# Kernel optimization log

Hardware: AMD Instinct MI355X
Metric: run time of the kernel (lower is better)

Reference implementation:

```python
import jax, jax.numpy as jnp
import numpy as np

EMBED_DIM = 1024
NUM_HEADS = 16
HEAD_DIM = EMBED_DIM // NUM_HEADS


def setup_inputs() -> dict:
    key = jax.random.key(0)
    ks = jax.random.split(key, 7)
    B, S, D = 2, 2048, EMBED_DIM
    scale = 1.0 / np.sqrt(D)
    return {
        "query": jax.random.normal(ks[0], (B, S, D), dtype=jnp.float32),
        "key": jax.random.normal(ks[1], (B, S, D), dtype=jnp.float32),
        "value": jax.random.normal(ks[2], (B, S, D), dtype=jnp.float32),
        "W_qkv": jax.random.normal(ks[3], (D, 3 * D), dtype=jnp.float32) * scale,
        "b_qkv": jnp.zeros((3 * D,), dtype=jnp.float32),
        "W_out": jax.random.normal(ks[4], (D, D), dtype=jnp.float32) * scale,
        "b_out": jnp.zeros((D,), dtype=jnp.float32),
    }


def reference(query, key, value, W_qkv, b_qkv, W_out, b_out):
    # NOTE: the original torch forward ignores `key` and `value` — q,k,v all
    # come from qkv_proj(query). We keep them as args for signature fidelity.
    B, S, D = query.shape
    H, hd = NUM_HEADS, HEAD_DIM
    scale = hd ** -0.5

    qkv = query @ W_qkv + b_qkv                      # [B, S, 3D]
    qkv = qkv.reshape(B, S, 3, H, hd)
    q = jnp.transpose(qkv[:, :, 0], (0, 2, 1, 3))    # [B, H, S, hd]
    k = jnp.transpose(qkv[:, :, 1], (0, 2, 1, 3))
    v = jnp.transpose(qkv[:, :, 2], (0, 2, 1, 3))

    scores = jnp.einsum("bhsd,bhtd->bhst", q, k) * scale  # [B, H, S, S]
    attn = jax.nn.softmax(scores, axis=-1)
    out = jnp.einsum("bhst,bhtd->bhsd", attn, v)           # [B, H, S, hd]
    out = jnp.transpose(out, (0, 2, 1, 3)).reshape(B, S, D)
    return out @ W_out + b_out
```

## Files before the change

kernel.cpp:

```cpp
#include <hip/hip_runtime.h>
#include <stdint.h>

#define DEV static __device__ __forceinline__

typedef __attribute__((ext_vector_type(4))) float f32x4;
typedef __attribute__((ext_vector_type(16))) float f32x16;
typedef __attribute__((ext_vector_type(8))) short bf16x8;
typedef bf16x8 __attribute__((may_alias)) bf16x8_a;
typedef __attribute__((ext_vector_type(2))) unsigned int u32x2;
typedef u32x2 __attribute__((may_alias)) u32x2_a;

DEV unsigned short f2bf(float f) {
  union { float f; unsigned int u; } v; v.f = f;
  return (unsigned short)((v.u + 0x7FFFu + ((v.u >> 16) & 1u)) >> 16);
}

DEV float bf2f(unsigned short s) {
  union { unsigned int u; float f; } v; v.u = ((unsigned int)s) << 16;
  return v.f;
}

DEV float fast_exp2(float x) {
  float r;
  asm("v_exp_f32 %0, %1" : "=v"(r) : "v"(x));
  return r;
}

DEV unsigned int pktrunc(float lo, float hi) {
  union { float f; unsigned int u; } a, b; a.f = lo; b.f = hi;
  return __builtin_amdgcn_perm(b.u, a.u, 0x07060302u);
}

DEV void gload_lds16(const void* g, void* l) {
  __builtin_amdgcn_global_load_lds(
      (const __attribute__((address_space(1))) unsigned int*)g,
      (__attribute__((address_space(3))) unsigned int*)l, 16, 0, 0);
}

__global__ void cast_bf16_k(const float4* __restrict__ in, ushort4* __restrict__ out, int n4) {
  int i = blockIdx.x * 256 + threadIdx.x;
  if (i >= n4) return;
  float4 f = in[i];
  ushort4 o; o.x = f2bf(f.x); o.y = f2bf(f.y); o.z = f2bf(f.z); o.w = f2bf(f.w);
  out[i] = o;
}

__global__ __launch_bounds__(256) void transpose_bf16_k(const float* __restrict__ in,
                                                        unsigned short* __restrict__ out,
                                                        int R, int C) {
  __shared__ float tile[32][33];
  const int t = threadIdx.x;
  const int r = t >> 3, c4 = (t & 7) << 2;
  const int tr = blockIdx.y << 5, tc = blockIdx.x << 5;
  const float4 v = *(const float4*)(in + (size_t)(tr + r) * C + tc + c4);
  tile[r][c4] = v.x; tile[r][c4 + 1] = v.y; tile[r][c4 + 2] = v.z; tile[r][c4 + 3] = v.w;
  __syncthreads();
  ushort4 o;
  o.x = f2bf(tile[c4][r]); o.y = f2bf(tile[c4 + 1][r]);
  o.z = f2bf(tile[c4 + 2][r]); o.w = f2bf(tile[c4 + 3][r]);
  *(ushort4*)(out + (size_t)(tc + r) * R + tr + c4) = o;
}

template <int EPI, int BN>
__global__ __launch_bounds__(256) void gemm_bt(const unsigned short* __restrict__ A,
                                               const unsigned short* __restrict__ BT,
                                               const float* __restrict__ bias,
                                               float* __restrict__ Cout,
                                               unsigned short* __restrict__ q_buf,
                                               unsigned short* __restrict__ k_buf,
                                               unsigned short* __restrict__ vT_buf,
                                               int M, int N, int K) {
  constexpr int MI = (BN == 128) ? 4 : 2;
  constexpr int MW = MI * 16;
  __shared__ unsigned short As[2][128 * 32];
  __shared__ unsigned short Bs[2][BN * 32];
  const int t = threadIdx.x, w = t >> 6, l = t & 63;
  const int wm = (BN == 128) ? (w >> 1) : w;
  const int wn = (BN == 128) ? (w & 1) : 0;
  const int lg = l >> 4, ln = l & 15;

  const int xcd = blockIdx.x & 7, jb = blockIdx.x >> 3;
  const int m0 = (xcd * 4 + (jb & 3)) * 128;
  const int n0 = (jb >> 2) * BN;

  const int srow = w * 16 + (l >> 2);
  const int schunk = (l & 3) ^ ((l >> 3) & 3);
  const int dchunk = l & 3;

  f32x4 acc[MI][4] = {};

#define STAGE_G(buf, k0)                                                                              \
  do {                                                                                                \
    gload_lds16(A + (size_t)(m0 + srow) * K + (k0) + schunk * 8, &As[buf][srow * 32 + dchunk * 8]);   \
    gload_lds16(A + (size_t)(m0 + srow + 64) * K + (k0) + schunk * 8,                                 \
                &As[buf][(srow + 64) * 32 + dchunk * 8]);                                             \
    gload_lds16(BT + (size_t)(n0 + srow) * K + (k0) + schunk * 8, &Bs[buf][srow * 32 + dchunk * 8]);  \
    if (BN == 128)                                                                                    \
      gload_lds16(BT + (size_t)(n0 + srow + 64) * K + (k0) + schunk * 8,                              \
                  &Bs[buf][(srow + 64) * 32 + dchunk * 8]);                                           \
  } while (0)

  STAGE_G(0, 0);
  __syncthreads();

  const int rsw = (ln >> 1) & 3;
  const int rchunk = (lg ^ rsw) << 3;
  const int nit = K >> 5;
  for (int it = 0; it < nit; ++it) {
    const int buf = it & 1;
    if (it + 1 < nit) STAGE_G(buf ^ 1, (it + 1) * 32);

    bf16x8 af[MI], bfr[4];
#pragma unroll
    for (int mi = 0; mi < MI; ++mi)
      af[mi] = *(const bf16x8_a*)&As[buf][(wm * MW + mi * 16 + ln) * 32 + rchunk];
#pragma unroll
    for (int ni = 0; ni < 4; ++ni)
      bfr[ni] = *(const bf16x8_a*)&Bs[buf][(wn * 64 + ni * 16 + ln) * 32 + rchunk];
#pragma unroll
    for (int mi = 0; mi < MI; ++mi)
#pragma unroll
      for (int ni = 0; ni < 4; ++ni)
        acc[mi][ni] = __builtin_amdgcn_mfma_f32_16x16x32_bf16(af[mi], bfr[ni], acc[mi][ni], 0, 0, 0);

    __syncthreads();
  }
#undef STAGE_G

#pragma unroll
  for (int ni = 0; ni < 4; ++ni) {
    const int c = n0 + wn * 64 + ni * 16 + ln;
    const float bv = bias[c];
    if (EPI == 1) {
      const int which = c >> 10;
      const int h = (c >> 6) & 15;
      const int d = c & 63;
#pragma unroll
      for (int mi = 0; mi < MI; ++mi) {
        const int mrow = m0 + wm * MW + mi * 16 + lg * 4;
        const int b = mrow >> 11, s = mrow & 2047;
        const size_t bh = (size_t)(b * 16 + h);
        f32x4 v = acc[mi][ni];
        if (which == 0) {
          const float QSCALE = 0.125f * 1.44269504088896340736f;
          unsigned short* dst = q_buf + (bh * 2048 + s) * 64 + d;
#pragma unroll
          for (int r = 0; r < 4; ++r) dst[(size_t)r * 64] = f2bf((v[r] + bv) * QSCALE);
        } else if (which == 1) {
          unsigned short* dst = k_buf + (bh * 2048 + s) * 64 + d;
#pragma unroll
          for (int r = 0; r < 4; ++r) dst[(size_t)r * 64] = f2bf(v[r] + bv);
        } else {
          const int sp = (s & ~12) | ((s & 4) << 1) | ((s & 8) >> 1);
          unsigned short* dst = vT_buf + (bh * 64 + d) * 2048 + sp;
          ushort4 o4;
          o4.x = f2bf(v[0] + bv); o4.y = f2bf(v[1] + bv); o4.z = f2bf(v[2] + bv); o4.w = f2bf(v[3] + bv);
          *(ushort4*)dst = o4;
        }
      }
    } else {
#pragma unroll
      for (int mi = 0; mi < MI; ++mi) {
        const int mrow = m0 + wm * MW + mi * 16 + lg * 4;
        f32x4 v = acc[mi][ni];
#pragma unroll
        for (int r = 0; r < 4; ++r) Cout[(size_t)(mrow + r) * N + c] = v[r] + bv;
      }
    }
  }
}

template <int SPLIT>
__global__ __launch_bounds__(256, 4) void attn_k(const unsigned short* __restrict__ Qb,
                                                 const unsigned short* __restrict__ Kb,
                                                 const unsigned short* __restrict__ Vt,
                                                 unsigned short* __restrict__ AO,
                                                 unsigned short* __restrict__ Opart,
                                                 float* __restrict__ lpart) {
  constexpr int NT = 32 / SPLIT;
  const float SHIFT = -15.9943754f;
  const float CINV  = 0.99610895f;
  __shared__ unsigned short Ks[2][64 * 64];
  __shared__ unsigned short Vs[2][64 * 64];

  const int t = threadIdx.x, w = t >> 6, l = t & 63;
  const int l31 = l & 31, lh = l >> 5;
  const int xcd = blockIdx.x & 7, idx = blockIdx.x >> 3;
  const int bh = xcd * 4 + (idx & 3);
  const int qt = (SPLIT == 2) ? ((idx >> 2) & 15) : (idx >> 2);
  const int half = (SPLIT == 2) ? (idx >> 6) : 0;
  const int b = bh >> 4, h = bh & 15;
  const unsigned short* Q = Qb + (size_t)bh * 2048 * 64;
  const unsigned short* K = Kb + (size_t)bh * 2048 * 64 + (size_t)half * NT * 64 * 64;
  const unsigned short* V = Vt + (size_t)bh * 64 * 2048 + half * NT * 64;
  const int qbase = qt * 128 + w * 32;

  const int srow = t >> 3;
  const int scol = ((t & 7) ^ (srow & 7)) << 3;
  const int dcol = (t & 7) << 3;

  bf16x8 qf[4];
#pragma unroll
  for (int kd = 0; kd < 4; ++kd)
    qf[kd] = *(const bf16x8_a*)(Q + (size_t)(qbase + l31) * 64 + kd * 16 + lh * 8);

  f32x16 o32[2] = {};
  float lr = 0.f;

  {
    gload_lds16(K + (size_t)srow * 64 + scol,        &Ks[0][srow * 64 + dcol]);
    gload_lds16(K + (size_t)(srow + 32) * 64 + scol, &Ks[0][(srow + 32) * 64 + dcol]);
    gload_lds16(V + (size_t)srow * 2048 + scol,        &Vs[0][srow * 64 + dcol]);
    gload_lds16(V + (size_t)(srow + 32) * 2048 + scol, &Vs[0][(srow + 32) * 64 + dcol]);
  }
  __syncthreads();

  for (int tk = 0; tk < NT; ++tk) {
    const int cur = tk & 1;
    if (tk < NT - 1) {
      const int k1 = (tk + 1) * 64;
      const unsigned short* Kg = K + (size_t)k1 * 64;
      const unsigned short* Vg = V + k1;
      gload_lds16(Kg + (size_t)srow * 64 + scol,        &Ks[cur ^ 1][srow * 64 + dcol]);
      gload_lds16(Kg + (size_t)(srow + 32) * 64 + scol, &Ks[cur ^ 1][(srow + 32) * 64 + dcol]);
      gload_lds16(Vg + (size_t)srow * 2048 + scol,        &Vs[cur ^ 1][srow * 64 + dcol]);
      gload_lds16(Vg + (size_t)(srow + 32) * 2048 + scol, &Vs[cur ^ 1][(srow + 32) * 64 + dcol]);
    }

    f32x16 sa[2] = {};
#pragma unroll
    for (int m2 = 0; m2 < 2; ++m2)
#pragma unroll
      for (int kd = 0; kd < 4; ++kd) {
        const bf16x8 kf = *(const bf16x8_a*)
            &Ks[cur][(m2 * 32 + l31) * 64 + (((kd * 2 + lh) ^ (l & 7)) << 3)];
        sa[m2] = __builtin_amdgcn_mfma_f32_32x32x16_bf16(kf, qf[kd], sa[m2], 0, 0, 0);
      }

    bf16x8 vf0[4];
#pragma unroll
    for (int ksI = 0; ksI < 4; ++ksI)
      vf0[ksI] = *(const bf16x8_a*)&Vs[cur][l31 * 64 + (((ksI * 2 + lh) ^ (l & 7)) << 3)];

    unsigned int pk[2][8];
    float rs = 0.f;
#pragma unroll
    for (int m2 = 0; m2 < 2; ++m2) {
      float p[16];
#pragma unroll
      for (int r = 0; r < 16; ++r) {
        p[r] = fast_exp2(sa[m2][r] + SHIFT);
        rs += p[r];
      }
#pragma unroll
      for (int u = 0; u < 8; ++u)
        pk[m2][u] = pktrunc(p[2 * u], p[2 * u + 1]);
    }
    rs += __shfl_xor(rs, 32);
    lr += rs;

#pragma unroll
    for (int m2 = 0; m2 < 2; ++m2)
#pragma unroll
      for (int ks2 = 0; ks2 < 2; ++ks2) {
        const int ksI = m2 * 2 + ks2;
        union { unsigned int u[4]; bf16x8 v; } pa;
        pa.u[0] = pk[m2][ks2 * 4 + 0];
        pa.u[1] = pk[m2][ks2 * 4 + 1];
        pa.u[2] = pk[m2][ks2 * 4 + 2];
        pa.u[3] = pk[m2][ks2 * 4 + 3];
        const bf16x8 vf1 = *(const bf16x8_a*)
            &Vs[cur][(32 + l31) * 64 + (((ksI * 2 + lh) ^ (l & 7)) << 3)];
        o32[0] = __builtin_amdgcn_mfma_f32_32x32x16_bf16(pa.v, vf0[ksI], o32[0], 0, 0, 0);
        o32[1] = __builtin_amdgcn_mfma_f32_32x32x16_bf16(pa.v, vf1, o32[1], 0, 0, 0);
      }

    __syncthreads();
  }

  lr *= CINV;

  if (SPLIT == 2) {
    const size_t pbase = ((size_t)(half * 32 + bh) * 2048 + qbase);
#pragma unroll
    for (int nb = 0; nb < 2; ++nb)
#pragma unroll
      for (int r = 0; r < 16; ++r) {
        const int qrow = (r & 3) + 8 * (r >> 2) + 4 * lh;
        Opart[(pbase + qrow) * 64 + nb * 32 + l31] = f2bf(o32[nb][r]);
      }
    if (l < 32) lpart[pbase + l] = lr;
  } else {
    const float inv = 1.0f / lr;
    float iv[16];
#pragma unroll
    for (int r = 0; r < 16; ++r)
      iv[r] = __shfl(inv, (r & 3) + 8 * (r >> 2) + 4 * lh);
#pragma unroll
    for (int nb = 0; nb < 2; ++nb)
#pragma unroll
      for (int r = 0; r < 16; ++r) {
        const int qrow = (r & 3) + 8 * (r >> 2) + 4 * lh;
        const size_t row = (size_t)b * 2048 + qbase + qrow;
        AO[row * 1024 + h * 64 + nb * 32 + l31] = f2bf(o32[nb][r] * iv[r]);
      }
  }
}

__global__ __launch_bounds__(256) void merge_k(const unsigned short* __restrict__ Opart,
                                               const float* __restrict__ lpart,
                                               unsigned short* __restrict__ AO) {
  const int u = blockIdx.x * 256 + threadIdx.x;
  const int c8 = u & 7, s = (u >> 3) & 2047, bh = u >> 14;
  const int b = bh >> 4, h = bh & 15;
  const size_t r0 = (size_t)bh * 2048 + s;
  const size_t r1 = (size_t)(32 + bh) * 2048 + s;
  const bf16x8 a0 = *(const bf16x8_a*)(Opart + r0 * 64 + c8 * 8);
  const bf16x8 a1 = *(const bf16x8_a*)(Opart + r1 * 64 + c8 * 8);
  const float inv = 1.0f / (lpart[r0] + lpart[r1]);
  bf16x8 oo;
#pragma unroll
  for (int i = 0; i < 8; ++i)
    oo[i] = (short)f2bf((bf2f((unsigned short)a0[i]) + bf2f((unsigned short)a1[i])) * inv);
  *(bf16x8_a*)(AO + ((size_t)b * 2048 + s) * 1024 + h * 64 + c8 * 8) = oo;
}

extern "C" void kernel_launch(void* const* d_in, const int* in_sizes, int n_in,
                              void* d_out, int out_size, void* d_ws, size_t ws_size,
                              hipStream_t stream) {
  const float* query = (const float*)d_in[0];
  const float* W_qkv = (const float*)d_in[3];
  const float* b_qkv = (const float*)d_in[4];
  const float* W_out = (const float*)d_in[5];
  const float* b_out = (const float*)d_in[6];
  float* out = (float*)d_out;
  char* ws = (char*)d_ws;

  unsigned short* Xb    = (unsigned short*)(ws);
  unsigned short* WqkvT = (unsigned short*)(ws + 8388608);
  unsigned short* WoutT = (unsigned short*)(ws + 14680064);
  unsigned short* qb    = (unsigned short*)(ws + 16777216);
  unsigned short* kb    = (unsigned short*)(ws + 25165824);
  unsigned short* vT    = (unsigned short*)(ws + 33554432);
  unsigned short* Opart = (unsigned short*)(ws + 41943040);
  float*          lpart = (float*)(ws + 58720256);
  const bool split2 = ws_size >= 59244544;
  unsigned short* AO    = Xb;

  cast_bf16_k<<<4096, 256, 0, stream>>>((const float4*)query, (ushort4*)Xb, 1048576);
  transpose_bf16_k<<<dim3(96, 32), 256, 0, stream>>>(W_qkv, WqkvT, 1024, 3072);
  transpose_bf16_k<<<dim3(32, 32), 256, 0, stream>>>(W_out, WoutT, 1024, 1024);
  gemm_bt<1, 128><<<768, 256, 0, stream>>>(Xb, WqkvT, b_qkv, nullptr, qb, kb, vT, 4096, 3072, 1024);
  if (split2) {
    attn_k<2><<<1024, 256, 0, stream>>>(qb, kb, vT, nullptr, Opart, lpart);
    merge_k<<<2048, 256, 0, stream>>>(Opart, lpart, AO);
  } else {
    attn_k<1><<<512, 256, 0, stream>>>(qb, kb, vT, AO, nullptr, nullptr);
  }
  gemm_bt<0, 64><<<512, 256, 0, stream>>>(AO, WoutT, b_out, out, nullptr, nullptr, nullptr, 4096, 1024, 1024);
}
```

Before: 123.0 us.

## Fuse prep kernels, shrink QKV GEMM tile, and read V fragments directly from global

Merges the bf16 cast and two weight transposes into one prep kernel to cut launch overhead. The QKV GEMM moves to 64-row M tiles with launch bounds of 6, doubling the block count for better occupancy and load balance. The attention kernel drops the LDS staging of V and loads V fragments straight from global memory into registers, halving LDS traffic and footprint. The risk is that uncoalesced global V reads stall the MFMA pipeline and that smaller GEMM tiles lower data reuse.

Result: slower. 149.3 us (+21.3%).

```diff
diff --git a/kernel.cpp b/kernel.cpp
--- a/kernel.cpp
+++ b/kernel.cpp
@@ -37,21 +37,10 @@
       (__attribute__((address_space(3))) unsigned int*)l, 16, 0, 0);
 }
 
-__global__ void cast_bf16_k(const float4* __restrict__ in, ushort4* __restrict__ out, int n4) {
-  int i = blockIdx.x * 256 + threadIdx.x;
-  if (i >= n4) return;
-  float4 f = in[i];
-  ushort4 o; o.x = f2bf(f.x); o.y = f2bf(f.y); o.z = f2bf(f.z); o.w = f2bf(f.w);
-  out[i] = o;
-}
-
-__global__ __launch_bounds__(256) void transpose_bf16_k(const float* __restrict__ in,
-                                                        unsigned short* __restrict__ out,
-                                                        int R, int C) {
-  __shared__ float tile[32][33];
-  const int t = threadIdx.x;
+DEV void transpose_body(const float* __restrict__ in, unsigned short* __restrict__ out,
+                        int R, int C, int bx, int by, int t, float (*tile)[33]) {
   const int r = t >> 3, c4 = (t & 7) << 2;
-  const int tr = blockIdx.y << 5, tc = blockIdx.x << 5;
+  const int tr = by << 5, tc = bx << 5;
   const float4 v = *(const float4*)(in + (size_t)(tr + r) * C + tc + c4);
   tile[r][c4] = v.x; tile[r][c4 + 1] = v.y; tile[r][c4 + 2] = v.z; tile[r][c4 + 3] = v.w;
   __syncthreads();
@@ -61,39 +50,65 @@
   *(ushort4*)(out + (size_t)(tc + r) * R + tr + c4) = o;
 }
 
-template <int EPI, int BN>
-__global__ __launch_bounds__(256) void gemm_bt(const unsigned short* __restrict__ A,
-                                               const unsigned short* __restrict__ BT,
-                                               const float* __restrict__ bias,
-                                               float* __restrict__ Cout,
-                                               unsigned short* __restrict__ q_buf,
-                                               unsigned short* __restrict__ k_buf,
-                                               unsigned short* __restrict__ vT_buf,
-                                               int M, int N, int K) {
-  constexpr int MI = (BN == 128) ? 4 : 2;
+__global__ __launch_bounds__(256) void prep_k(const float4* __restrict__ q4,
+                                              ushort4* __restrict__ Xb,
+                                              const float* __restrict__ Wqkv,
+                                              unsigned short* __restrict__ WqkvT,
+                                              const float* __restrict__ Wout,
+                                              unsigned short* __restrict__ WoutT) {
+  __shared__ float tile[32][33];
+  const int t = threadIdx.x, bid = blockIdx.x;
+  if (bid < 4096) {
+    const int i = bid * 256 + t;
+    float4 f = q4[i];
+    ushort4 o; o.x = f2bf(f.x); o.y = f2bf(f.y); o.z = f2bf(f.z); o.w = f2bf(f.w);
+    Xb[i] = o;
+  } else if (bid < 4096 + 3072) {
+    const int id = bid - 4096;
+    transpose_body(Wqkv, WqkvT, 1024, 3072, id % 96, id / 96, t, tile);
+  } else {
+    const int id = bid - 4096 - 3072;
+    transpose_body(Wout, WoutT, 1024, 1024, id & 31, id >> 5, t, tile);
+  }
+}
+
+template <int EPI, int BN, int TM>
+__global__ __launch_bounds__(256, 6) void gemm_bt(const unsigned short* __restrict__ A,
+                                                  const unsigned short* __restrict__ BT,
+                                                  const float* __restrict__ bias,
+                                                  float* __restrict__ Cout,
+                                                  unsigned short* __restrict__ q_buf,
+                                                  unsigned short* __restrict__ k_buf,
+                                                  unsigned short* __restrict__ vT_buf,
+                                                  int M, int N, int K) {
+  constexpr int NWM = (TM == 64) ? 2 : ((BN == 128) ? 2 : 4);
+  constexpr int NWN = 4 / NWM;
+  constexpr int MI = TM / NWM / 16;
   constexpr int MW = MI * 16;
-  __shared__ unsigned short As[2][128 * 32];
+  __shared__ unsigned short As[2][TM * 32];
   __shared__ unsigned short Bs[2][BN * 32];
   const int t = threadIdx.x, w = t >> 6, l = t & 63;
-  const int wm = (BN == 128) ? (w >> 1) : w;
-  const int wn = (BN == 128) ? (w & 1) : 0;
+  const int wm = (NWM == 2) ? (w >> 1) : w;
+  const int wn = (NWN == 2) ? (w & 1) : 0;
   const int lg = l >> 4, ln = l & 15;
 
   const int xcd = blockIdx.x & 7, jb = blockIdx.x >> 3;
-  const int m0 = (xcd * 4 + (jb & 3)) * 128;
-  const int n0 = (jb >> 2) * BN;
-
-  const int srow = w * 16 + (l >> 2);
-  const int schunk = (l & 3) ^ ((l >> 3) & 3);
-  const int dchunk = l & 3;
+  const int per_xcd = (M / TM) >> 3;
+  const int m0 = (xcd * per_xcd + (jb % per_xcd)) * TM;
+  const int n0 = (jb / per_xcd) * BN;
+
+  const int srow = t >> 2;
+  const int schunk = (t & 3) ^ ((t >> 3) & 3);
+  const int dchunk = t & 3;
 
   f32x4 acc[MI][4] = {};
 
 #define STAGE_G(buf, k0)                                                                              \
   do {                                                                                                \
     gload_lds16(A + (size_t)(m0 + srow) * K + (k0) + schunk * 8, &As[buf][srow * 32 + dchunk * 8]);   \
-    gload_lds16(A + (size_t)(m0 + srow + 64) * K + (k0) + schunk * 8,                                 \
-                &As[buf][(srow + 64) * 32 + dchunk * 8]);                                             \
+    if (TM == 128)                                                                                    \
+      gload_lds16(A + (size_t)(m0 + srow + 64) * K + (k0) + schunk * 8,                               \
+                  &As[buf][(srow + 64) * 32 + dchunk * 8]);                                           \
     gload_lds16(BT + (size_t)(n0 + srow) * K + (k0) + schunk * 8, &Bs[buf][srow * 32 + dchunk * 8]);  \
     if (BN == 128)                                                                                    \
       gload_lds16(BT + (size_t)(n0 + srow + 64) * K + (k0) + schunk * 8,                              \
@@ -103,8 +118,7 @@
   STAGE_G(0, 0);
   __syncthreads();
 
-  const int rsw = (ln >> 1) & 3;
-  const int rchunk = (lg ^ rsw) << 3;
+  const int rchunk = (lg ^ ((ln >> 1) & 3)) << 3;
   const int nit = K >> 5;
   for (int it = 0; it < nit; ++it) {
     const int buf = it & 1;
@@ -181,9 +195,8 @@
   const float SHIFT = -15.9943754f;
   const float CINV  = 0.99610895f;
   __shared__ unsigned short Ks[2][64 * 64];
-  __shared__ unsigned short Vs[2][64 * 64];
-
-  const int t = threadIdx.x, w = t >> 6, l = t & 63;
+
+  const int t = threadIdx.x, l = t & 63;
   const int l31 = l & 31, lh = l >> 5;
   const int xcd = blockIdx.x & 7, idx = blockIdx.x >> 3;
   const int bh = xcd * 4 + (idx & 3);
@@ -193,7 +206,7 @@
   const unsigned short* Q = Qb + (size_t)bh * 2048 * 64;
   const unsigned short* K = Kb + (size_t)bh * 2048 * 64 + (size_t)half * NT * 64 * 64;
   const unsigned short* V = Vt + (size_t)bh * 64 * 2048 + half * NT * 64;
-  const int qbase = qt * 128 + w * 32;
+  const int qbase = qt * 128 + (t >> 6) * 32;
 
   const int srow = t >> 3;
   const int scol = ((t & 7) ^ (srow & 7)) << 3;
@@ -210,22 +223,22 @@
   {
     gload_lds16(K + (size_t)srow * 64 + scol,        &Ks[0][srow * 64 + dcol]);
     gload_lds16(K + (size_t)(srow + 32) * 64 + scol, &Ks[0][(srow + 32) * 64 + dcol]);
-    gload_lds16(V + (size_t)srow * 2048 + scol,        &Vs[0][srow * 64 + dcol]);
-    gload_lds16(V + (size_t)(srow + 32) * 2048 + scol, &Vs[0][(srow + 32) * 64 + dcol]);
   }
   __syncthreads();
 
   for (int tk = 0; tk < NT; ++tk) {
     const int cur = tk & 1;
+    const int k0 = tk * 64;
     if (tk < NT - 1) {
-      const int k1 = (tk + 1) * 64;
-      const unsigned short* Kg = K + (size_t)k1 * 64;
-      const unsigned short* Vg = V + k1;
+      const unsigned short* Kg = K + (size_t)(k0 + 64) * 64;
       gload_lds16(Kg + (size_t)srow * 64 + scol,        &Ks[cur ^ 1][srow * 64 + dcol]);
       gload_lds16(Kg + (size_t)(srow + 32) * 64 + scol, &Ks[cur ^ 1][(srow + 32) * 64 + dcol]);
-      gload_lds16(Vg + (size_t)srow * 2048 + scol,        &Vs[cur ^ 1][srow * 64 + dcol]);
-      gload_lds16(Vg + (size_t)(srow + 32) * 2048 + scol, &Vs[cur ^ 1][(srow + 32) * 64 + dcol]);
     }
+
+    bf16x8 vf0[4];
+#pragma unroll
+    for (int ksI = 0; ksI < 4; ++ksI)
+      vf0[ksI] = *(const bf16x8_a*)(V + (size_t)l31 * 2048 + k0 + ksI * 16 + lh * 8);
 
     f32x16 sa[2] = {};
 #pragma unroll
@@ -236,11 +249,6 @@
             &Ks[cur][(m2 * 32 + l31) * 64 + (((kd * 2 + lh) ^ (l & 7)) << 3)];
         sa[m2] = __builtin_amdgcn_mfma_f32_32x32x16_bf16(kf, qf[kd], sa[m2], 0, 0, 0);
       }
-
-    bf16x8 vf0[4];
-#pragma unroll
-    for (int ksI = 0; ksI < 4; ++ksI)
-      vf0[ksI] = *(const bf16x8_a*)&Vs[cur][l31 * 64 + (((ksI * 2 + lh) ^ (l & 7)) << 3)];
 
     unsigned int pk[2][8];
     float rs = 0.f;
@@ -259,21 +267,26 @@
     rs += __shfl_xor(rs, 32);
     lr += rs;
 
+    bf16x8 vf1[4];
+#pragma unroll
+    for (int ksI = 0; ksI < 4; ++ksI)
+      vf1[ksI] = *(const bf16x8_a*)(V + (size_t)(32 + l31) * 2048 + k0 + ksI * 16 + lh * 8);
+
+    union { unsigned int u[4]; bf16x8 v; } pa[4];
 #pragma unroll
     for (int m2 = 0; m2 < 2; ++m2)
 #pragma unroll
       for (int ks2 = 0; ks2 < 2; ++ks2) {
         const int ksI = m2 * 2 + ks2;
-        union { unsigned int u[4]; bf16x8 v; } pa;
-        pa.u[0] = pk[m2][ks2 * 4 + 0];
-        pa.u[1] = pk[m2][ks2 * 4 + 1];
-        pa.u[2] = pk[m2][ks2 * 4 + 2];
-        pa.u[3] = pk[m2][ks2 * 4 + 3];
-        const bf16x8 vf1 = *(const bf16x8_a*)
-            &Vs[cur][(32 + l31) * 64 + (((ksI * 2 + lh) ^ (l & 7)) << 3)];
-        o32[0] = __builtin_amdgcn_mfma_f32_32x32x16_bf16(pa.v, vf0[ksI], o32[0], 0, 0, 0);
-        o32[1] = __builtin_amdgcn_mfma_f32_32x32x16_bf16(pa.v, vf1, o32[1], 0, 0, 0);
-      }
+        pa[ksI].u[0] = pk[m2][ks2 * 4 + 0];
+        pa[ksI].u[1] = pk[m2][ks2 * 4 + 1];
+        pa[ksI].u[2] = pk[m2][ks2 * 4 + 2];
+        pa[ksI].u[3] = pk[m2][ks2 * 4 + 3];
+        o32[0] = __builtin_amdgcn_mfma_f32_32x32x16_bf16(pa[ksI].v, vf0[ksI], o32[0], 0, 0, 0);
+      }
+#pragma unroll
+    for (int ksI = 0; ksI < 4; ++ksI)
+      o32[1] = __builtin_amdgcn_mfma_f32_32x32x16_bf16(pa[ksI].v, vf1[ksI], o32[1], 0, 0, 0);
 
     __syncthreads();
   }
@@ -347,15 +360,16 @@
   const bool split2 = ws_size >= 59244544;
   unsigned short* AO    = Xb;
 
-  cast_bf16_k<<<4096, 256, 0, stream>>>((const float4*)query, (ushort4*)Xb, 1048576);
-  transpose_bf16_k<<<dim3(96, 32), 256, 0, stream>>>(W_qkv, WqkvT, 1024, 3072);
-  transpose_bf16_k<<<dim3(32, 32), 256, 0, stream>>>(W_out, WoutT, 1024, 1024);
-  gemm_bt<1, 128><<<768, 256, 0, stream>>>(Xb, WqkvT, b_qkv, nullptr, qb, kb, vT, 4096, 3072, 1024);
+  prep_k<<<8192, 256, 0, stream>>>((const float4*)query, (ushort4*)Xb,
+                                   W_qkv, WqkvT, W_out, WoutT);
+  gemm_bt<1, 128, 64><<<1536, 256, 0, stream>>>(Xb, WqkvT, b_qkv, nullptr, qb, kb, vT,
+                                                4096, 3072, 1024);
   if (split2) {
     attn_k<2><<<1024, 256, 0, stream>>>(qb, kb, vT, nullptr, Opart, lpart);
     merge_k<<<2048, 256, 0, stream>>>(Opart, lpart, AO);
   } else {
     attn_k<1><<<512, 256, 0, stream>>>(qb, kb, vT, AO, nullptr, nullptr);
   }
-  gemm_bt<0, 64><<<512, 256, 0, stream>>>(AO, WoutT, b_out, out, nullptr, nullptr, nullptr, 4096, 1024, 1024);
-}
+  gemm_bt<0, 64, 128><<<512, 256, 0, stream>>>(AO, WoutT, b_out, out, nullptr, nullptr, nullptr,
+                                               4096, 1024, 1024);
+}
```
